# Kernel optimization log

Hardware: AMD Instinct MI355X
Metric: run time of the kernel (lower is better)

Reference implementation:

```python
import jax, jax.numpy as jnp
import numpy as np

TWN_THRESHOLD_FACTOR = 0.05
BN_EPS = 1e-5


def ternary_quantize(w):
    # threshold = 0.05 * max|w| (detached); q in {-1, 0, +1}
    t = TWN_THRESHOLD_FACTOR * jnp.max(jnp.abs(jax.lax.stop_gradient(w)))
    return (w > t).astype(w.dtype) - (w < -t).astype(w.dtype)


def conv2d(x, w, b):
    q = ternary_quantize(w)
    y = jax.lax.conv_general_dilated(x, q, (1, 1), 'VALID',
                                     dimension_numbers=('NCHW', 'OIHW', 'NCHW'))
    return y + b[None, :, None, None]


def linear(x, w, b):
    q = ternary_quantize(w)
    return x @ q.T + b


def bn_train(x, gamma, beta, axes):
    # training-mode batch norm (biased variance), matches torch BN in train()
    mean = jnp.mean(x, axis=axes, keepdims=True)
    var = jnp.var(x, axis=axes, keepdims=True)
    xhat = (x - mean) * jax.lax.rsqrt(var + BN_EPS)
    shape = [1] * x.ndim
    shape[1] = x.shape[1]
    return xhat * gamma.reshape(shape) + beta.reshape(shape)


def maxpool2(x):
    return jax.lax.reduce_window(x, -jnp.inf, jax.lax.max,
                                 (1, 1, 2, 2), (1, 1, 2, 2), 'VALID')


def setup_inputs() -> dict:
    key = jax.random.key(0)
    ks = jax.random.split(key, 8)
    B, Cin, H, W = 512, 1, 28, 28
    C1, C2, K = 64, 128, 5
    FLAT, F1, F2 = 4 * 4 * C2, 512, 10
    inp = {
        'x': jax.random.normal(ks[0], (B, Cin, H, W), jnp.float32),
        'conv1_w': jax.random.normal(ks[1], (C1, Cin, K, K), jnp.float32) * (1.0 / np.sqrt(Cin * K * K)),
        'conv1_b': jax.random.normal(ks[2], (C1,), jnp.float32) * 0.05,
        'bn1_g': jnp.ones((C1,), jnp.float32),
        'bn1_b': jnp.zeros((C1,), jnp.float32),
        'conv2_w': jax.random.normal(ks[3], (C2, C1, K, K), jnp.float32) * (1.0 / np.sqrt(C1 * K * K)),
        'conv2_b': jax.random.normal(ks[4], (C2,), jnp.float32) * 0.05,
        'bn2_g': jnp.ones((C2,), jnp.float32),
        'bn2_b': jnp.zeros((C2,), jnp.float32),
        'fc1_w': jax.random.normal(ks[5], (F1, FLAT), jnp.float32) * (1.0 / np.sqrt(FLAT)),
        'fc1_b': jax.random.normal(ks[6], (F1,), jnp.float32) * 0.05,
        'bn3_g': jnp.ones((F1,), jnp.float32),
        'bn3_b': jnp.zeros((F1,), jnp.float32),
        'fc2_w': jax.random.normal(ks[7], (F2, F1), jnp.float32) * (1.0 / np.sqrt(F1)),
        'fc2_b': jnp.zeros((F2,), jnp.float32),
    }
    return inp


def reference(x, conv1_w, conv1_b, bn1_g, bn1_b, conv2_w, conv2_b, bn2_g, bn2_b,
              fc1_w, fc1_b, bn3_g, bn3_b, fc2_w, fc2_b):
    h = jax.nn.relu(bn_train(conv2d(x, conv1_w, conv1_b), bn1_g, bn1_b, (0, 2, 3)))
    h = maxpool2(h)  # [B, 64, 12, 12]
    h = jax.nn.relu(bn_train(conv2d(h, conv2_w, conv2_b), bn2_g, bn2_b, (0, 2, 3)))
    h = maxpool2(h)  # [B, 128, 4, 4]
    h = h.reshape(h.shape[0], -1)  # [B, 2048]
    h = jax.nn.relu(bn_train(linear(h, fc1_w, fc1_b), bn3_g, bn3_b, (0,)))
    return linear(h, fc2_w, fc2_b)  # [B, 10]
```

## Files before the change

### kernel.cpp

```cpp
#include <hip/hip_runtime.h>
#include <stdint.h>

#define EPS 1e-5f

typedef short v8s __attribute__((ext_vector_type(8)));
typedef float v4f __attribute__((ext_vector_type(4)));

static const size_t W2F   = 8192;
static const size_t WF2F  = 212992;
static const size_t A_F   = 262144;
static const size_t PMN2F = 4980736;
static const size_t B_F   = 19136512;
static const size_t WF1T  = B_F + 1048576;

#define P_C1 1024
#define P_F2 1025
#define P_C2 1040
#define P_F1 1240

__device__ inline unsigned short f2bf(float f) {
    unsigned u = __float_as_uint(f);
    return (unsigned short)((u + 0x7FFF + ((u >> 16) & 1)) >> 16);
}

__global__ void k_absz(const float* __restrict__ c1w, const float* __restrict__ c2w,
                       const float* __restrict__ f1w, const float* __restrict__ f2w,
                       float* __restrict__ wsf) {
    __shared__ float sm4[4];
    int blk = blockIdx.x;
    if (blk >= 384) {
        if (blk < 386) {
            int i = (blk - 384) * 256 + threadIdx.x + 16;
            if (i < 528) wsf[i] = 0.f;
        } else {
            int i = (blk - 386) * 256 + threadIdx.x + 1808;
            if (i < 2832) wsf[i] = 0.f;
        }
        return;
    }
    const float* w; int n; int nb; int bi; float* out;
    if (blk == 0)       { w = c1w; n = 1600;    nb = 1;   bi = 0;         out = wsf + P_C1; }
    else if (blk == 1)  { w = f2w; n = 5120;    nb = 1;   bi = 0;         out = wsf + P_F2; }
    else if (blk < 194) { w = c2w; n = 204800;  nb = 192; bi = blk - 2;   out = wsf + P_C2 + bi; }
    else                { w = f1w; n = 1048576; nb = 190; bi = blk - 194; out = wsf + P_F1 + bi; }
    float m = 0.f;
    for (int i = bi * 256 + threadIdx.x; i < n; i += nb * 256)
        m = fmaxf(m, fabsf(w[i]));
    #pragma unroll
    for (int o = 32; o; o >>= 1) m = fmaxf(m, __shfl_down(m, o));
    if ((threadIdx.x & 63) == 0) sm4[threadIdx.x >> 6] = m;
    __syncthreads();
    if (threadIdx.x == 0)
        *out = fmaxf(fmaxf(sm4[0], sm4[1]), fmaxf(sm4[2], sm4[3]));
}

__global__ __launch_bounds__(512) void k_mid(const float* __restrict__ x,
                                             const float* __restrict__ c1w,
                                             const float* __restrict__ c2w,
                                             const float* __restrict__ f1w,
                                             const float* __restrict__ f2w,
                                             float* __restrict__ wsf,
                                             unsigned* __restrict__ pmn1,
                                             unsigned short* __restrict__ w2u,
                                             unsigned short* __restrict__ wf1,
                                             float* __restrict__ wf2) {
    int blk = blockIdx.x;
    int tid = threadIdx.x;
    if (blk >= 1024) {
        if (blk < 1124) {
            __shared__ float rm[8];
            float m = (tid < 192) ? wsf[P_C2 + tid] : 0.f;
            #pragma unroll
            for (int o = 32; o; o >>= 1) m = fmaxf(m, __shfl_down(m, o));
            if ((tid & 63) == 0) rm[tid >> 6] = m;
            __syncthreads();
            float t = 0.05f * fmaxf(fmaxf(rm[0], rm[1]), rm[2]);
            for (int i = (blk - 1024) * 512 + tid; i < 204800; i += 100 * 512) {
                int j    = i & 7;
                int lane = (i >> 3) & 63;
                int mt   = (i >> 9) & 7;
                int ks   = (i >> 12) & 1;
                int p    = i >> 13;
                int c  = mt * 16 + (lane & 15);
                int ci = ks * 32 + (lane >> 4) * 8 + j;
                float v = c2w[c * 1600 + ci * 25 + p];
                w2u[i] = (v > t) ? (unsigned short)0x3F80
                                 : ((v < -t) ? (unsigned short)0xBF80 : (unsigned short)0);
            }
        } else if (blk < 1380) {
            __shared__ float rm[8];
            float m = (tid < 190) ? wsf[P_F1 + tid] : 0.f;
            #pragma unroll
            for (int o = 32; o; o >>= 1) m = fmaxf(m, __shfl_down(m, o));
            if ((tid & 63) == 0) rm[tid >> 6] = m;
            __syncthreads();
            float t = 0.05f * fmaxf(fmaxf(rm[0], rm[1]), rm[2]);
            for (int i = (blk - 1124) * 512 + tid; i < 1048576; i += 256 * 512) {
                float v = f1w[i];
                unsigned short q = (v > t) ? (unsigned short)0x3F80
                                 : ((v < -t) ? (unsigned short)0xBF80 : (unsigned short)0);
                int f = i >> 11, k = i & 2047;
                int ft = f >> 4, fm = f & 15;
                int ks = k >> 5, kr = k & 31;
                int lane = (kr >> 3) * 16 + fm;
                wf1[((size_t)(ks * 32 + ft) * 64 + lane) * 8 + (kr & 7)] = q;
            }
        } else {
            float t = 0.05f * wsf[P_F2];
            for (int i = tid; i < 5120; i += 512) {
                float v = f2w[i];
                wf2[i] = (float)((v > t) - (v < -t));
            }
        }
        return;
    }
    __shared__ float xs[448];
    __shared__ float red[2][8][64];
    int img  = blk >> 1;
    int half = blk & 1;
    const float4* xim = (const float4*)(x + (size_t)img * 784 + half * 336);
    for (int i = tid; i < 112; i += 512) ((float4*)xs)[i] = xim[i];
    int c  = tid & 63;
    int wv = tid >> 6;
    float w[25];
    {
        float t = 0.05f * wsf[P_C1];
        const float* src = c1w + c * 25;
        #pragma unroll
        for (int k = 0; k < 25; ++k) {
            float v = src[k];
            w[k] = (float)((v > t) - (v < -t));
        }
    }
    __syncthreads();
    unsigned* ob = pmn1 + (size_t)img * 9216;
    float s = 0.f, s2 = 0.f;
    int lph = 0, pw = wv;
    for (int it = 0; it < 9; ++it) {
        const float* xp = xs + (lph * 2) * 28 + pw * 2;
        float win[36];
        #pragma unroll
        for (int i = 0; i < 6; ++i)
            #pragma unroll
            for (int j = 0; j < 3; ++j) {
                float2 t2 = *(const float2*)(xp + i * 28 + j * 2);
                win[i * 6 + j * 2] = t2.x; win[i * 6 + j * 2 + 1] = t2.y;
            }
        float v00 = 0.f, v01 = 0.f, v10 = 0.f, v11 = 0.f;
        #pragma unroll
        for (int i = 0; i < 5; ++i)
            #pragma unroll
            for (int j = 0; j < 5; ++j) {
                float wk = w[i * 5 + j];
                v00 = fmaf(win[i * 6 + j],           wk, v00);
                v01 = fmaf(win[i * 6 + j + 1],       wk, v01);
                v10 = fmaf(win[(i + 1) * 6 + j],     wk, v10);
                v11 = fmaf(win[(i + 1) * 6 + j + 1], wk, v11);
            }
        s  += v00 + v01 + v10 + v11;
        s2 += v00 * v00 + v01 * v01 + v10 * v10 + v11 * v11;
        float mx = fmaxf(fmaxf(v00, v01), fmaxf(v10, v11));
        float mn = fminf(fminf(v00, v01), fminf(v10, v11));
        ob[((half * 6 + lph) * 12 + pw) * 64 + c] = ((unsigned)f2bf(mx) << 16) | (unsigned)f2bf(mn);
        pw += 8; if (pw >= 12) { pw -= 12; ++lph; }
    }
    red[0][wv][c] = s; red[1][wv][c] = s2;
    __syncthreads();
    if (tid < 64) {
        float S = 0.f, S2 = 0.f;
        #pragma unroll
        for (int i = 0; i < 8; ++i) { S += red[0][i][tid]; S2 += red[1][i][tid]; }
        atomicAdd(&wsf[16 + tid], S);
        atomicAdd(&wsf[80 + tid], S2);
    }
}

__global__ __launch_bounds__(256) void k_conv2(const unsigned* __restrict__ pmn1,
                                               const unsigned short* __restrict__ wfrag,
                                               const float* __restrict__ c1sum,
                                               const float* __restrict__ c1ssq,
                                               const float* __restrict__ g1,
                                               const float* __restrict__ b1,
                                               float* __restrict__ pmn,
                                               float* __restrict__ sum,
                                               float* __restrict__ ssq) {
    __shared__ unsigned short xs[2][10944];
    __shared__ float reds[2][64], redq[2][64];
    int pair  = blockIdx.x >> 1;
    int mhalf = blockIdx.x & 1;
    int tid  = threadIdx.x;
    int lane = tid & 63;
    int wave = tid >> 6;
    int nh = wave & 1, kp = wave >> 1;

    int ch0 = (tid & 15) * 4;
    float scv[4], shv[4];
    {
        const float invN = 1.f / 294912.f;
        #pragma unroll
        for (int j = 0; j < 4; ++j) {
            int ch = ch0 + j;
            float mean = c1sum[ch] * invN;
            float var  = c1ssq[ch] * invN - mean * mean;
            scv[j] = g1[ch] * rsqrtf(var + EPS);
            shv[j] = b1[ch] - mean * scv[j];
        }
    }
    #pragma unroll
    for (int ii = 0; ii < 2; ++ii) {
        const uint4* srcp = (const uint4*)(pmn1 + (size_t)(pair * 2 + ii) * 9216);
        unsigned short* xsi = &xs[ii][0];
        for (int it = 0; it < 9; ++it) {
            int i = it * 256 + tid;
            int r = i >> 4;
            uint4 u4 = srcp[i];
            unsigned long long pack = 0;
            #pragma unroll
            for (int j = 0; j < 4; ++j) {
                unsigned u = (&u4.x)[j];
                float mx = __uint_as_float(u & 0xffff0000u);
                float mn = __uint_as_float(u << 16);
                float v = (scv[j] > 0.f) ? mx : mn;
                unsigned short o = f2bf(fmaxf(0.f, fmaf(v, scv[j], shv[j])));
                pack |= ((unsigned long long)o) << (16 * j);
            }
            *(unsigned long long*)(&xsi[r * 76 + ch0]) = pack;
        }
    }
    __syncthreads();

    int n = lane & 15, quad = lane >> 4;
    int ow = n & 7;
    int ohb0 = nh * 4 + (n >> 3);
    int col0 = kp * 32 + quad * 8;
    v4f acc[2][4][2];
    #pragma unroll
    for (int ii = 0; ii < 2; ++ii)
        #pragma unroll
        for (int mm = 0; mm < 4; ++mm) {
            acc[ii][mm][0] = (v4f){0,0,0,0};
            acc[ii][mm][1] = (v4f){0,0,0,0};
        }
    for (int p = 0; p < 25; ++p) {
        int kh = p / 5, kw = p - (p / 5) * 5;
        int col = (ow + kw) * 76 + col0;
        v8s bfA0 = *(const v8s*)(&xs[0][(ohb0 + kh) * 912 + col]);
        v8s bfA1 = *(const v8s*)(&xs[0][(ohb0 + 2 + kh) * 912 + col]);
        v8s bfB0 = *(const v8s*)(&xs[1][(ohb0 + kh) * 912 + col]);
        v8s bfB1 = *(const v8s*)(&xs[1][(ohb0 + 2 + kh) * 912 + col]);
        #pragma unroll
        for (int mm = 0; mm < 4; ++mm) {
            v8s af = *(const v8s*)(wfrag +
                (size_t)((p * 2 + kp) * 8 + mhalf * 4 + mm) * 512 + lane * 8);
            acc[0][mm][0] = __builtin_amdgcn_mfma_f32_16x16x32_bf16(af, bfA0, acc[0][mm][0], 0, 0, 0);
            acc[0][mm][1] = __builtin_amdgcn_mfma_f32_16x16x32_bf16(af, bfA1, acc[0][mm][1], 0, 0, 0);
            acc[1][mm][0] = __builtin_amdgcn_mfma_f32_16x16x32_bf16(af, bfB0, acc[1][mm][0], 0, 0, 0);
            acc[1][mm][1] = __builtin_amdgcn_mfma_f32_16x16x32_bf16(af, bfB1, acc[1][mm][1], 0, 0, 0);
        }
    }
    __syncthreads();
    float* mbuf = (float*)xs;
    if (kp == 1) {
        #pragma unroll
        for (int ii = 0; ii < 2; ++ii) {
            float* d = mbuf + ii * 4608 + (nh * 64 + lane) * 36;
            #pragma unroll
            for (int mm = 0; mm < 4; ++mm) {
                *(v4f*)(d + mm * 8)     = acc[ii][mm][0];
                *(v4f*)(d + mm * 8 + 4) = acc[ii][mm][1];
            }
        }
    }
    __syncthreads();
    if (kp == 0) {
        #pragma unroll
        for (int ii = 0; ii < 2; ++ii) {
            const float* s = mbuf + ii * 4608 + (nh * 64 + lane) * 36;
            #pragma unroll
            for (int mm = 0; mm < 4; ++mm) {
                acc[ii][mm][0] += *(const v4f*)(s + mm * 8);
                acc[ii][mm][1] += *(const v4f*)(s + mm * 8 + 4);
            }
        }
        float* po0 = pmn + (size_t)(pair * 2 + 0) * 4096;
        float* po1 = pmn + (size_t)(pair * 2 + 1) * 4096;
        #pragma unroll
        for (int mm = 0; mm < 4; ++mm) {
            int cl0 = mm * 16 + quad * 4;
            #pragma unroll
            for (int r = 0; r < 4; ++r) {
                int cl = cl0 + r;
                int cc = mhalf * 64 + cl;
                float sA = 0.f, s2A = 0.f;
                #pragma unroll
                for (int ii = 0; ii < 2; ++ii) {
                    float* po = ii ? po1 : po0;
                    #pragma unroll
                    for (int bf = 0; bf < 2; ++bf) {
                        float v = acc[ii][mm][bf][r];
                        float pm = fmaxf(v, __shfl_xor(v, 1));
                        float pn = fminf(v, __shfl_xor(v, 1));
                        pm = fmaxf(pm, __shfl_xor(pm, 8));
                        pn = fminf(pn, __shfl_xor(pn, 8));
                        if (((n & 1) == 0) && (n < 8)) {
                            int psp = (nh * 2 + bf) * 4 + (n >> 1);
                            *(float2*)(&po[(cc * 16 + psp) * 2]) = make_float2(pm, pn);
                        }
                        float s = v, s2 = v * v;
                        #pragma unroll
                        for (int m = 1; m < 16; m <<= 1) { s += __shfl_xor(s, m); s2 += __shfl_xor(s2, m); }
                        sA += s; s2A += s2;
                    }
                }
                if (n == 0) { reds[nh][cl] = sA; redq[nh][cl] = s2A; }
            }
        }
    }
    __syncthreads();
    if (tid < 64) {
        atomicAdd(&sum[mhalf * 64 + tid], reds[0][tid] + reds[1][tid]);
        atomicAdd(&ssq[mhalf * 64 + tid], redq[0][tid] + redq[1][tid]);
    }
}

__global__ void k_bnpool2(const float* __restrict__ pmn2, const float* __restrict__ c2sum,
                          const float* __restrict__ c2ssq, const float* __restrict__ g2,
                          const float* __restrict__ b2, unsigned short* __restrict__ xfrag) {
    int i = blockIdx.x * 256 + threadIdx.x;
    int j    = i & 7;
    int lane = (i >> 3) & 63;
    int bt   = (i >> 9) & 31;
    int ks   = i >> 14;
    int b = bt * 16 + (lane & 15);
    int k = ks * 32 + (lane >> 4) * 8 + j;
    int c = k >> 4, psp = k & 15;
    float2 mm = *(const float2*)(&pmn2[((size_t)b * 2048 + c * 16 + psp) * 2]);
    float mean = c2sum[c] * (1.f / 32768.f);
    float var  = c2ssq[c] * (1.f / 32768.f) - mean * mean;
    float sc = g2[c] * rsqrtf(var + EPS);
    float sh = b2[c] - mean * sc;
    float v = (sc > 0.f) ? mm.x : mm.y;
    xfrag[i] = f2bf(fmaxf(0.f, fmaf(v, sc, sh)));
}

__global__ __launch_bounds__(256) void k_fc1(const unsigned short* __restrict__ xfrag,
                                             const unsigned short* __restrict__ wfrag,
                                             float* __restrict__ out,
                                             float* __restrict__ sum,
                                             float* __restrict__ ssq) {
    int lane = threadIdx.x & 63;
    int wave = threadIdx.x >> 6;
    int ft = (blockIdx.x & 7) * 4 + wave;
    int bT = blockIdx.x >> 3;
    v4f acc = (v4f){0.f, 0.f, 0.f, 0.f};
    for (int ks = 0; ks < 64; ++ks) {
        v8s bfrag = *(const v8s*)(xfrag + ((size_t)(ks * 32 + bT) * 64 + lane) * 8);
        v8s afrag = *(const v8s*)(wfrag + ((size_t)(ks * 32 + ft) * 64 + lane) * 8);
        acc = __builtin_amdgcn_mfma_f32_16x16x32_bf16(afrag, bfrag, acc, 0, 0, 0);
    }
    int bb = bT * 16 + (lane & 15);
    int quad = lane >> 4;
    int f0 = ft * 16 + quad * 4;
    *(float4*)(&out[(size_t)bb * 512 + f0]) =
        make_float4(acc[0], acc[1], acc[2], acc[3]);
    #pragma unroll
    for (int r = 0; r < 4; ++r) {
        float s = acc[r], s2 = s * s;
        #pragma unroll
        for (int m = 1; m < 16; m <<= 1) { s += __shfl_xor(s, m); s2 += __shfl_xor(s2, m); }
        if ((lane & 15) == 0) { atomicAdd(&sum[f0 + r], s); atomicAdd(&ssq[f0 + r], s2); }
    }
}

__global__ __launch_bounds__(256) void k_fc2(const float* __restrict__ x,
                                             const float* __restrict__ w,
                                             const float* __restrict__ bias,
                                             const float* __restrict__ fsum,
                                             const float* __restrict__ fssq,
                                             const float* __restrict__ g3,
                                             const float* __restrict__ b3,
                                             float* __restrict__ out) {
    int lane = threadIdx.x & 63;
    int b = blockIdx.x * 4 + (threadIdx.x >> 6);
    float xa[8], sm[8], sq[8], ga[8], ba[8];
    {
        const float4* p;
        p = (const float4*)(x + (size_t)b * 512 + lane * 8);
        *(float4*)xa = p[0]; *(float4*)(xa + 4) = p[1];
        p = (const float4*)(fsum + lane * 8);
        *(float4*)sm = p[0]; *(float4*)(sm + 4) = p[1];
        p = (const float4*)(fssq + lane * 8);
        *(float4*)sq = p[0]; *(float4*)(sq + 4) = p[1];
        p = (const float4*)(g3 + lane * 8);
        *(float4*)ga = p[0]; *(float4*)(ga + 4) = p[1];
        p = (const float4*)(b3 + lane * 8);
        *(float4*)ba = p[0]; *(float4*)(ba + 4) = p[1];
    }
    float h[8];
    #pragma unroll
    for (int e = 0; e < 8; ++e) {
        float mean = sm[e] * (1.f / 512.f);
        float var  = sq[e] * (1.f / 512.f) - mean * mean;
        float sc = ga[e] * rsqrtf(var + EPS);
        float sh = ba[e] - mean * sc;
        h[e] = fmaxf(0.f, fmaf(xa[e], sc, sh));
    }
    #pragma unroll
    for (int j = 0; j < 10; ++j) {
        const float4* wp = (const float4*)(w + j * 512 + lane * 8);
        float4 w0 = wp[0], w1 = wp[1];
        float p = h[0] * w0.x + h[1] * w0.y + h[2] * w0.z + h[3] * w0.w
                + h[4] * w1.x + h[5] * w1.y + h[6] * w1.z + h[7] * w1.w;
        #pragma unroll
        for (int o = 32; o; o >>= 1) p += __shfl_down(p, o);
        if (lane == 0) out[b * 10 + j] = p + bias[j];
    }
}

extern "C" void kernel_launch(void* const* d_in, const int* in_sizes, int n_in,
                              void* d_out, int out_size, void* d_ws, size_t ws_size,
                              hipStream_t stream) {
    const float* x       = (const float*)d_in[0];
    const float* conv1_w = (const float*)d_in[1];
    const float* bn1_g   = (const float*)d_in[3];
    const float* bn1_b   = (const float*)d_in[4];
    const float* conv2_w = (const float*)d_in[5];
    const float* bn2_g   = (const float*)d_in[7];
    const float* bn2_b   = (const float*)d_in[8];
    const float* fc1_w   = (const float*)d_in[9];
    const float* bn3_g   = (const float*)d_in[11];
    const float* bn3_b   = (const float*)d_in[12];
    const float* fc2_w   = (const float*)d_in[13];
    const float* fc2_b   = (const float*)d_in[14];

    float* wsf = (float*)d_ws;

    float* c1_sum = wsf + 16,   * c1_ssq = wsf + 80;
    float* c2_sum = wsf + 272,  * c2_ssq = wsf + 400;
    float* f_sum  = wsf + 1808, * f_ssq  = wsf + 2320;

    unsigned short* w2u = (unsigned short*)(wsf + W2F);
    float* wf2 = wsf + WF2F;
    unsigned short* wf1 = (unsigned short*)(wsf + WF1T);
    unsigned* PMN1 = (unsigned*)(wsf + A_F);
    float* PMN2 = wsf + PMN2F;
    float* A    = wsf + A_F;
    unsigned short* xfrag = (unsigned short*)(wsf + B_F);

    k_absz<<<390, 256, 0, stream>>>(conv1_w, conv2_w, fc1_w, fc2_w, wsf);

    k_mid<<<1381, 512, 0, stream>>>(x, conv1_w, conv2_w, fc1_w, fc2_w, wsf,
                                    PMN1, w2u, wf1, wf2);

    k_conv2<<<512, 256, 0, stream>>>(PMN1, (const unsigned short*)w2u,
                                     c1_sum, c1_ssq, bn1_g, bn1_b,
                                     PMN2, c2_sum, c2_ssq);

    k_bnpool2<<<4096, 256, 0, stream>>>(PMN2, c2_sum, c2_ssq, bn2_g, bn2_b, xfrag);

    k_fc1<<<256, 256, 0, stream>>>(xfrag, wf1, A, f_sum, f_ssq);

    k_fc2<<<128, 256, 0, stream>>>(A, wf2, fc2_b, f_sum, f_ssq, bn3_g, bn3_b,
                                   (float*)d_out);
}
```

Measured before the change: 188.7 us.

## Process one image per conv2 block and double the grid for occupancy

Each conv2 block used to handle a pair of images. It now handles a single image, and the grid doubles to 1024 blocks. The block-to-image mapping is reordered so that the two output-channel halves of the same eight images sit on nearby block indices. This halves shared memory and accumulator registers per block, and with launch_bounds(256,4) more blocks can be resident per CU. The cost is that each weight fragment is reused across half as many MFMAs, so global/L2 weight traffic doubles and the fully unrolled p-loop grows code size.

```diff
diff --git a/kernel.cpp b/kernel.cpp
--- a/kernel.cpp
+++ b/kernel.cpp
@@ -175,19 +175,20 @@
     }
 }
 
-__global__ __launch_bounds__(256) void k_conv2(const unsigned* __restrict__ pmn1,
-                                               const unsigned short* __restrict__ wfrag,
-                                               const float* __restrict__ c1sum,
-                                               const float* __restrict__ c1ssq,
-                                               const float* __restrict__ g1,
-                                               const float* __restrict__ b1,
-                                               float* __restrict__ pmn,
-                                               float* __restrict__ sum,
-                                               float* __restrict__ ssq) {
-    __shared__ unsigned short xs[2][10944];
+__global__ __launch_bounds__(256, 4) void k_conv2(const unsigned* __restrict__ pmn1,
+                                                  const unsigned short* __restrict__ wfrag,
+                                                  const float* __restrict__ c1sum,
+                                                  const float* __restrict__ c1ssq,
+                                                  const float* __restrict__ g1,
+                                                  const float* __restrict__ b1,
+                                                  float* __restrict__ pmn,
+                                                  float* __restrict__ sum,
+                                                  float* __restrict__ ssq) {
+    __shared__ unsigned short xs[10944];
     __shared__ float reds[2][64], redq[2][64];
-    int pair  = blockIdx.x >> 1;
-    int mhalf = blockIdx.x & 1;
+    int b = blockIdx.x;
+    int img   = (b >> 4) * 8 + (b & 7);
+    int mhalf = (b >> 3) & 1;
     int tid  = threadIdx.x;
     int lane = tid & 63;
     int wave = tid >> 6;
@@ -206,26 +207,23 @@
             shv[j] = b1[ch] - mean * scv[j];
         }
     }
-    #pragma unroll
-    for (int ii = 0; ii < 2; ++ii) {
-        const uint4* srcp = (const uint4*)(pmn1 + (size_t)(pair * 2 + ii) * 9216);
-        unsigned short* xsi = &xs[ii][0];
-        for (int it = 0; it < 9; ++it) {
-            int i = it * 256 + tid;
-            int r = i >> 4;
-            uint4 u4 = srcp[i];
-            unsigned long long pack = 0;
-            #pragma unroll
-            for (int j = 0; j < 4; ++j) {
-                unsigned u = (&u4.x)[j];
-                float mx = __uint_as_float(u & 0xffff0000u);
-                float mn = __uint_as_float(u << 16);
-                float v = (scv[j] > 0.f) ? mx : mn;
-                unsigned short o = f2bf(fmaxf(0.f, fmaf(v, scv[j], shv[j])));
-                pack |= ((unsigned long long)o) << (16 * j);
-            }
-            *(unsigned long long*)(&xsi[r * 76 + ch0]) = pack;
-        }
+    const uint4* srcp = (const uint4*)(pmn1 + (size_t)img * 9216);
+    #pragma unroll
+    for (int it = 0; it < 9; ++it) {
+        int i = it * 256 + tid;
+        int r = i >> 4;
+        uint4 u4 = srcp[i];
+        unsigned long long pack = 0;
+        #pragma unroll
+        for (int j = 0; j < 4; ++j) {
+            unsigned u = (&u4.x)[j];
+            float mx = __uint_as_float(u & 0xffff0000u);
+            float mn = __uint_as_float(u << 16);
+            float v = (scv[j] > 0.f) ? mx : mn;
+            unsigned short o = f2bf(fmaxf(0.f, fmaf(v, scv[j], shv[j])));
+            pack |= ((unsigned long long)o) << (16 * j);
+        }
+        *(unsigned long long*)(&xs[r * 76 + ch0]) = pack;
     }
     __syncthreads();
 
@@ -233,57 +231,42 @@
     int ow = n & 7;
     int ohb0 = nh * 4 + (n >> 3);
     int col0 = kp * 32 + quad * 8;
-    v4f acc[2][4][2];
-    #pragma unroll
-    for (int ii = 0; ii < 2; ++ii)
-        #pragma unroll
-        for (int mm = 0; mm < 4; ++mm) {
-            acc[ii][mm][0] = (v4f){0,0,0,0};
-            acc[ii][mm][1] = (v4f){0,0,0,0};
-        }
+    v4f acc[4][2];
+    #pragma unroll
+    for (int mm = 0; mm < 4; ++mm) { acc[mm][0] = (v4f){0,0,0,0}; acc[mm][1] = (v4f){0,0,0,0}; }
+    const unsigned short* gw = wfrag + (size_t)(kp * 8 + mhalf * 4) * 512 + lane * 8;
+    #pragma unroll
     for (int p = 0; p < 25; ++p) {
         int kh = p / 5, kw = p - (p / 5) * 5;
         int col = (ow + kw) * 76 + col0;
-        v8s bfA0 = *(const v8s*)(&xs[0][(ohb0 + kh) * 912 + col]);
-        v8s bfA1 = *(const v8s*)(&xs[0][(ohb0 + 2 + kh) * 912 + col]);
-        v8s bfB0 = *(const v8s*)(&xs[1][(ohb0 + kh) * 912 + col]);
-        v8s bfB1 = *(const v8s*)(&xs[1][(ohb0 + 2 + kh) * 912 + col]);
+        v8s bf0 = *(const v8s*)(&xs[(ohb0 + kh) * 912 + col]);
+        v8s bf1 = *(const v8s*)(&xs[(ohb0 + 2 + kh) * 912 + col]);
         #pragma unroll
         for (int mm = 0; mm < 4; ++mm) {
-            v8s af = *(const v8s*)(wfrag +
-                (size_t)((p * 2 + kp) * 8 + mhalf * 4 + mm) * 512 + lane * 8);
-            acc[0][mm][0] = __builtin_amdgcn_mfma_f32_16x16x32_bf16(af, bfA0, acc[0][mm][0], 0, 0, 0);
-            acc[0][mm][1] = __builtin_amdgcn_mfma_f32_16x16x32_bf16(af, bfA1, acc[0][mm][1], 0, 0, 0);
-            acc[1][mm][0] = __builtin_amdgcn_mfma_f32_16x16x32_bf16(af, bfB0, acc[1][mm][0], 0, 0, 0);
-            acc[1][mm][1] = __builtin_amdgcn_mfma_f32_16x16x32_bf16(af, bfB1, acc[1][mm][1], 0, 0, 0);
+            v8s af = *(const v8s*)(gw + (size_t)p * 8192 + mm * 512);
+            acc[mm][0] = __builtin_amdgcn_mfma_f32_16x16x32_bf16(af, bf0, acc[mm][0], 0, 0, 0);
+            acc[mm][1] = __builtin_amdgcn_mfma_f32_16x16x32_bf16(af, bf1, acc[mm][1], 0, 0, 0);
         }
     }
     __syncthreads();
     float* mbuf = (float*)xs;
     if (kp == 1) {
-        #pragma unroll
-        for (int ii = 0; ii < 2; ++ii) {
-            float* d = mbuf + ii * 4608 + (nh * 64 + lane) * 36;
-            #pragma unroll
-            for (int mm = 0; mm < 4; ++mm) {
-                *(v4f*)(d + mm * 8)     = acc[ii][mm][0];
-                *(v4f*)(d + mm * 8 + 4) = acc[ii][mm][1];
-            }
+        float* d = mbuf + (nh * 64 + lane) * 36;
+        #pragma unroll
+        for (int mm = 0; mm < 4; ++mm) {
+            *(v4f*)(d + mm * 8)     = acc[mm][0];
+            *(v4f*)(d + mm * 8 + 4) = acc[mm][1];
         }
     }
     __syncthreads();
     if (kp == 0) {
-        #pragma unroll
-        for (int ii = 0; ii < 2; ++ii) {
-            const float* s = mbuf + ii * 4608 + (nh * 64 + lane) * 36;
-            #pragma unroll
-            for (int mm = 0; mm < 4; ++mm) {
-                acc[ii][mm][0] += *(const v4f*)(s + mm * 8);
-                acc[ii][mm][1] += *(const v4f*)(s + mm * 8 + 4);
-            }
-        }
-        float* po0 = pmn + (size_t)(pair * 2 + 0) * 4096;
-        float* po1 = pmn + (size_t)(pair * 2 + 1) * 4096;
+        const float* s = mbuf + (nh * 64 + lane) * 36;
+        #pragma unroll
+        for (int mm = 0; mm < 4; ++mm) {
+            acc[mm][0] += *(const v4f*)(s + mm * 8);
+            acc[mm][1] += *(const v4f*)(s + mm * 8 + 4);
+        }
+        float* po = pmn + (size_t)img * 4096;
         #pragma unroll
         for (int mm = 0; mm < 4; ++mm) {
             int cl0 = mm * 16 + quad * 4;
@@ -293,24 +276,20 @@
                 int cc = mhalf * 64 + cl;
                 float sA = 0.f, s2A = 0.f;
                 #pragma unroll
-                for (int ii = 0; ii < 2; ++ii) {
-                    float* po = ii ? po1 : po0;
+                for (int bf = 0; bf < 2; ++bf) {
+                    float v = acc[mm][bf][r];
+                    float pm = fmaxf(v, __shfl_xor(v, 1));
+                    float pn = fminf(v, __shfl_xor(v, 1));
+                    pm = fmaxf(pm, __shfl_xor(pm, 8));
+                    pn = fminf(pn, __shfl_xor(pn, 8));
+                    if (((n & 1) == 0) && (n < 8)) {
+                        int psp = (nh * 2 + bf) * 4 + (n >> 1);
+                        *(float2*)(&po[(cc * 16 + psp) * 2]) = make_float2(pm, pn);
+                    }
+                    float s = v, s2 = v * v;
                     #pragma unroll
-                    for (int bf = 0; bf < 2; ++bf) {
-                        float v = acc[ii][mm][bf][r];
-                        float pm = fmaxf(v, __shfl_xor(v, 1));
-                        float pn = fminf(v, __shfl_xor(v, 1));
-                        pm = fmaxf(pm, __shfl_xor(pm, 8));
-                        pn = fminf(pn, __shfl_xor(pn, 8));
-                        if (((n & 1) == 0) && (n < 8)) {
-                            int psp = (nh * 2 + bf) * 4 + (n >> 1);
-                            *(float2*)(&po[(cc * 16 + psp) * 2]) = make_float2(pm, pn);
-                        }
-                        float s = v, s2 = v * v;
-                        #pragma unroll
-                        for (int m = 1; m < 16; m <<= 1) { s += __shfl_xor(s, m); s2 += __shfl_xor(s2, m); }
-                        sA += s; s2A += s2;
-                    }
+                    for (int m = 1; m < 16; m <<= 1) { s += __shfl_xor(s, m); s2 += __shfl_xor(s2, m); }
+                    sA += s; s2A += s2;
                 }
                 if (n == 0) { reds[nh][cl] = sA; redq[nh][cl] = s2A; }
             }
@@ -452,9 +431,9 @@
     k_mid<<<1381, 512, 0, stream>>>(x, conv1_w, conv2_w, fc1_w, fc2_w, wsf,
                                     PMN1, w2u, wf1, wf2);
 
-    k_conv2<<<512, 256, 0, stream>>>(PMN1, (const unsigned short*)w2u,
-                                     c1_sum, c1_ssq, bn1_g, bn1_b,
-                                     PMN2, c2_sum, c2_ssq);
+    k_conv2<<<1024, 256, 0, stream>>>(PMN1, (const unsigned short*)w2u,
+                                      c1_sum, c1_ssq, bn1_g, bn1_b,
+                                      PMN2, c2_sum, c2_ssq);
 
     k_bnpool2<<<4096, 256, 0, stream>>>(PMN2, c2_sum, c2_ssq, bn2_g, bn2_b, xfrag);
 
```

After: 188.5 us. No clear change (-0.1%).
